# Optimization experiments

Measured on AMD Instinct MI355X. Metric: run time of the kernel, lower is better.

## Reference

```python
import jax, jax.numpy as jnp
import numpy as np

B, A, E = 8192, 56, 128          # batch, num_altas (=tgt_len), embed_dim
H, HD = 4, 16                     # num_heads, head_dim = E // H // 2
LAMBDA_INIT = 0.7
EPS = 1e-5
SCALING = HD ** -0.5


def _conv1d(x, w, b):
    # x: [N, C_in, L], w: [C_out, C_in, K], 'same' padding for K=7
    y = jax.lax.conv_general_dilated(
        x, w, window_strides=(1,), padding=[(3, 3)],
        dimension_numbers=('NCH', 'OIH', 'NCH'))
    return y + b[None, :, None]


def _layernorm(v, w, b):
    m = jnp.mean(v, axis=-1, keepdims=True)
    var = jnp.mean(jnp.square(v - m), axis=-1, keepdims=True)
    return (v - m) * jax.lax.rsqrt(var + EPS) * w + b


def setup_inputs() -> dict:
    key = jax.random.key(0)
    ks = jax.random.split(key, 12)
    return {
        'x': jax.random.normal(ks[0], (B, A, E), dtype=jnp.float32),
        'w_emb': jax.random.normal(ks[1], (A, A, 7), dtype=jnp.float32) * 0.05,
        'b_emb': jnp.zeros((A,), dtype=jnp.float32),
        'w_atlas': jax.random.normal(ks[2], (E, E, 7), dtype=jnp.float32) * 0.03,
        'b_atlas': jnp.zeros((E,), dtype=jnp.float32),
        'w_k': jax.random.normal(ks[3], (E, E), dtype=jnp.float32) * 0.08,
        'qn_w': jnp.ones((HD,), dtype=jnp.float32),
        'qn_b': jnp.zeros((HD,), dtype=jnp.float32),
        'kn_w': jnp.ones((HD,), dtype=jnp.float32),
        'kn_b': jnp.zeros((HD,), dtype=jnp.float32),
        'lambda_q1': jax.random.normal(ks[4], (HD,), dtype=jnp.float32) * 0.1,
        'lambda_k1': jax.random.normal(ks[5], (HD,), dtype=jnp.float32) * 0.1,
        'lambda_q2': jax.random.normal(ks[6], (HD,), dtype=jnp.float32) * 0.1,
        'lambda_k2': jax.random.normal(ks[7], (HD,), dtype=jnp.float32) * 0.1,
    }


def reference(x, w_emb, b_emb, w_atlas, b_atlas, w_k,
              qn_w, qn_b, kn_w, kn_b,
              lambda_q1, lambda_k1, lambda_q2, lambda_k2):
    bsz, tgt_len, embed_dim = x.shape
    # query formation: conv over atlas channels, SiLU, conv over embed channels,
    # SiLU, mean-pool over atlas positions -> [B, 1, E]
    h = jax.nn.silu(_conv1d(x, w_emb, b_emb))                  # [B, A, E]
    h = jax.nn.silu(_conv1d(h.transpose(0, 2, 1), w_atlas, b_atlas))  # [B, E, A]
    q = jnp.mean(h, axis=2)[:, None, :]                         # [B, 1, E]

    k = jnp.einsum('ble,oe->blo', x, w_k)                       # [B, A, E]

    q = q.reshape(bsz, 1, 2 * H, HD)
    k = k.reshape(bsz, tgt_len, 2 * H, HD)
    q = _layernorm(q, qn_w, qn_b) * SCALING
    k = _layernorm(k, kn_w, kn_b)

    attn = jnp.einsum('bqhe,bkhe->bhqk', q, k)                  # [B, 2H, 1, A]
    attn = jax.nn.softmax(attn, axis=-1)

    lam1 = jnp.exp(jnp.sum(lambda_q1 * lambda_k1))
    lam2 = jnp.exp(jnp.sum(lambda_q2 * lambda_k2))
    lambda_full = lam1 - lam2 + LAMBDA_INIT

    attn = attn.reshape(bsz, H, 2, 1, tgt_len)
    diff = attn[:, :, 0] - lambda_full * attn[:, :, 1]          # [B, H, 1, A]
    out = jax.nn.softmax(diff, axis=-1).mean(axis=1)            # [B, 1, A]
    return out.reshape(bsz, -1)                                 # [B, A]
```

## Files before the change

kernel.cpp:

```cpp
#include <hip/hip_runtime.h>
#include <math.h>

#define A_DIM 56
#define E_DIM 128

typedef short short8 __attribute__((ext_vector_type(8)));
typedef float floatx4 __attribute__((ext_vector_type(4)));

#define XT_HI_B 0
#define XT_LO_B 19296
#define H_HI_B  0
#define H_LO_B  16864
#define XR_HI_B 0
#define XR_LO_B 15232
#define KM_B    0
#define Q_B     33728
#define QN_B    34240
#define LG_B    34752
#define DP_B    36672
#define LAM_B   38592
#define SMEM_B  38608

#define QF   (Q_B/4)
#define QNF  (QN_B/4)
#define LGF  (LG_B/4)
#define DPF  (DP_B/4)
#define LAMF (LAM_B/4)
#define KP2  132

#define W1H 0
#define W1L 28672
#define W2H 57344
#define W2L 172032
#define WKH 286720
#define WKL 303104
#define PREP_ELEMS 159744

__device__ __forceinline__ unsigned rne16(unsigned u) {
  return (u + 0x7FFFu + ((u >> 16) & 1u)) >> 16;
}
__device__ __forceinline__ unsigned pack_hi16(unsigned u0, unsigned u1) {
  return __builtin_amdgcn_perm(u1, u0, 0x07060302u);
}
__device__ __forceinline__ float silu_f(float v) { return v / (1.f + __expf(-v)); }

__global__ void prep_weights(const float* __restrict__ w_emb,
                             const float* __restrict__ w_atlas,
                             const float* __restrict__ w_k,
                             unsigned short* __restrict__ ws) {
  int idx = blockIdx.x * 256 + threadIdx.x;
  if (idx >= PREP_ELEMS) return;
  float v; int dst_hi, dst_lo;
  if (idx < 28672) {
    int tap = idx >> 12, kc = (idx >> 11) & 1, nt = (idx >> 9) & 3;
    int lm = (idx >> 5) & 15, lkg = (idx >> 3) & 3, jj = idx & 7;
    int a = nt * 16 + lm, ci = kc * 32 + lkg * 8 + jj;
    v = (a < A_DIM && ci < A_DIM) ? w_emb[(a * A_DIM + ci) * 7 + tap] : 0.f;
    dst_hi = W1H + idx; dst_lo = W1L + idx;
  } else if (idx < 143360) {
    int j = idx - 28672;
    int tap = j >> 14, kc = (j >> 12) & 3, mt = (j >> 9) & 7;
    int lm = (j >> 5) & 15, lkg = (j >> 3) & 3, jj = j & 7;
    int eo = mt * 16 + lm, ei = kc * 32 + lkg * 8 + jj;
    v = w_atlas[(eo * E_DIM + ei) * 7 + tap];
    dst_hi = W2H + j; dst_lo = W2L + j;
  } else {
    int j = idx - 143360;
    int kc = j >> 12, mt = (j >> 9) & 7;
    int lm = (j >> 5) & 15, lkg = (j >> 3) & 3, jj = j & 7;
    int o = mt * 16 + lm, e = kc * 32 + lkg * 8 + jj;
    v = w_k[o * E_DIM + e];
    dst_hi = WKH + j; dst_lo = WKL + j;
  }
  unsigned u = __float_as_uint(v);
  unsigned hi = rne16(u);
  float lof = v - __uint_as_float(hi << 16);
  unsigned lo = rne16(__float_as_uint(lof));
  ws[dst_hi] = (unsigned short)hi;
  ws[dst_lo] = (unsigned short)lo;
}

__global__ __launch_bounds__(256, 4)
void atlas_fused(const float* __restrict__ x,
                 const unsigned short* __restrict__ ws,
                 const float* __restrict__ b_emb, const float* __restrict__ b_atlas,
                 const float* __restrict__ qn_w,  const float* __restrict__ qn_b,
                 const float* __restrict__ kn_w,  const float* __restrict__ kn_b,
                 const float* __restrict__ lq1,   const float* __restrict__ lk1,
                 const float* __restrict__ lq2,   const float* __restrict__ lk2,
                 float* __restrict__ out)
{
  __shared__ __align__(16) unsigned char smem[SMEM_B];
  float* smf = (float*)smem;
  const int t = threadIdx.x;
  const int b = blockIdx.x;
  const int lane = t & 63;
  const int w = __builtin_amdgcn_readfirstlane(t >> 6);
  const int lm = lane & 15;
  const int lkg8 = (lane >> 4) * 8;
  const int lr = (lane >> 4) * 4;

  const float* xb = x + (size_t)b * (A_DIM * E_DIM);

  {
    uint4 z4 = make_uint4(0, 0, 0, 0);
    for (int i = t; i < 352; i += 256) {
      if (i < 268) {
        int arr = i & 1, row = i >> 1;
        *(uint4*)(smem + (arr ? XT_LO_B : XT_HI_B) + row * 144 + 112) = z4;
      } else {
        int j = i - 268;
        int arr = j / 42; j -= arr * 42;
        int rowi = j / 7, c = j - rowi * 7;
        int row = (rowi < 3) ? rowi : 128 + rowi;
        *(uint4*)(smem + (arr ? XT_LO_B : XT_HI_B) + row * 144 + c * 16) = z4;
      }
    }
    if (t == 0) {
      float s1 = 0.f, s2 = 0.f;
      for (int i = 0; i < 16; ++i) { s1 += lq1[i] * lk1[i]; s2 += lq2[i] * lk2[i]; }
      smf[LAMF] = expf(s1) - expf(s2) + 0.7f;
    }
    int ab = t & 15;
    if (ab < 14) {
#pragma unroll
      for (int p = 0; p < 2; ++p) {
        int eb = (t >> 4) + 16 * p;
        floatx4 r0 = *(const floatx4*)(xb + (4 * ab + 0) * 128 + 4 * eb);
        floatx4 r1 = *(const floatx4*)(xb + (4 * ab + 1) * 128 + 4 * eb);
        floatx4 r2 = *(const floatx4*)(xb + (4 * ab + 2) * 128 + 4 * eb);
        floatx4 r3 = *(const floatx4*)(xb + (4 * ab + 3) * 128 + 4 * eb);
#pragma unroll
        for (int j2 = 0; j2 < 4; ++j2) {
          unsigned u0 = __float_as_uint(r0[j2]);
          unsigned u1 = __float_as_uint(r1[j2]);
          unsigned u2 = __float_as_uint(r2[j2]);
          unsigned u3 = __float_as_uint(r3[j2]);
          float l0 = r0[j2] - __uint_as_float(u0 & 0xFFFF0000u);
          float l1 = r1[j2] - __uint_as_float(u1 & 0xFFFF0000u);
          float l2 = r2[j2] - __uint_as_float(u2 & 0xFFFF0000u);
          float l3 = r3[j2] - __uint_as_float(u3 & 0xFFFF0000u);
          int off = (4 * eb + j2 + 3) * 144 + 8 * ab;
          *(uint2*)(smem + XT_HI_B + off) =
              make_uint2(pack_hi16(u0, u1), pack_hi16(u2, u3));
          *(uint2*)(smem + XT_LO_B + off) =
              make_uint2(pack_hi16(__float_as_uint(l0), __float_as_uint(l1)),
                         pack_hi16(__float_as_uint(l2), __float_as_uint(l3)));
        }
      }
    }
  }
  __syncthreads();

  {
    floatx4 acc[2][4];
#pragma unroll
    for (int nt = 0; nt < 4; ++nt) {
      int a = nt * 16 + lm;
      float be = (a < A_DIM) ? b_emb[a] : 0.f;
#pragma unroll
      for (int mt = 0; mt < 2; ++mt) {
        acc[mt][nt][0] = be; acc[mt][nt][1] = be;
        acc[mt][nt][2] = be; acc[mt][nt][3] = be;
      }
    }
    const unsigned short* xh = (const unsigned short*)(smem + XT_HI_B);
    const unsigned short* xl = (const unsigned short*)(smem + XT_LO_B);
#pragma unroll 1
    for (int tap = 0; tap < 7; ++tap) {
      int arow0 = (32 * w + lm + tap) * 72;
      int arow1 = arow0 + 16 * 72;
#pragma unroll
      for (int kc = 0; kc < 2; ++kc) {
        int ko = kc * 32 + lkg8;
        const unsigned short* fb = ws + ((tap * 2 + kc) * 4) * 512 + lm * 32 + lkg8;
        short8 bh0 = *(const short8*)(fb + W1H);
        short8 bh1 = *(const short8*)(fb + W1H + 512);
        short8 bh2 = *(const short8*)(fb + W1H + 1024);
        short8 bh3 = *(const short8*)(fb + W1H + 1536);
        short8 bl0 = *(const short8*)(fb + W1L);
        short8 bl1 = *(const short8*)(fb + W1L + 512);
        short8 bl2 = *(const short8*)(fb + W1L + 1024);
        short8 bl3 = *(const short8*)(fb + W1L + 1536);
        short8 ah0 = *(const short8*)(xh + arow0 + ko);
        short8 ah1 = *(const short8*)(xh + arow1 + ko);
        short8 al0 = *(const short8*)(xl + arow0 + ko);
        short8 al1 = *(const short8*)(xl + arow1 + ko);
        short8 bh[4] = {bh0, bh1, bh2, bh3};
        short8 bl[4] = {bl0, bl1, bl2, bl3};
#pragma unroll
        for (int nt = 0; nt < 4; ++nt) {
          acc[0][nt] = __builtin_amdgcn_mfma_f32_16x16x32_bf16(ah0, bh[nt], acc[0][nt], 0, 0, 0);
          acc[0][nt] = __builtin_amdgcn_mfma_f32_16x16x32_bf16(al0, bh[nt], acc[0][nt], 0, 0, 0);
          acc[0][nt] = __builtin_amdgcn_mfma_f32_16x16x32_bf16(ah0, bl[nt], acc[0][nt], 0, 0, 0);
          acc[1][nt] = __builtin_amdgcn_mfma_f32_16x16x32_bf16(ah1, bh[nt], acc[1][nt], 0, 0, 0);
          acc[1][nt] = __builtin_amdgcn_mfma_f32_16x16x32_bf16(al1, bh[nt], acc[1][nt], 0, 0, 0);
          acc[1][nt] = __builtin_amdgcn_mfma_f32_16x16x32_bf16(ah1, bl[nt], acc[1][nt], 0, 0, 0);
        }
      }
    }
    __syncthreads();
    {
      uint4 z4 = make_uint4(0, 0, 0, 0);
      for (int i = t; i < 204; i += 256) {
        int arr = i / 102, j = i - arr * 102;
        int r6 = j / 17, c = j - r6 * 17;
        int row = (r6 < 3) ? r6 : 56 + r6;
        *(uint4*)(smem + (arr ? H_LO_B : H_HI_B) + row * 272 + c * 16) = z4;
      }
    }
#pragma unroll
    for (int mt = 0; mt < 2; ++mt) {
      int e0 = 16 * (2 * w + mt) + lr;
#pragma unroll
      for (int nt = 0; nt < 4; ++nt) {
        int a = 16 * nt + lm;
        if (a < A_DIM) {
          float v0 = silu_f(acc[mt][nt][0]), v1 = silu_f(acc[mt][nt][1]);
          float v2 = silu_f(acc[mt][nt][2]), v3 = silu_f(acc[mt][nt][3]);
          unsigned u0 = __float_as_uint(v0), u1 = __float_as_uint(v1);
          unsigned u2 = __float_as_uint(v2), u3 = __float_as_uint(v3);
          float l0 = v0 - __uint_as_float(u0 & 0xFFFF0000u);
          float l1 = v1 - __uint_as_float(u1 & 0xFFFF0000u);
          float l2 = v2 - __uint_as_float(u2 & 0xFFFF0000u);
          float l3 = v3 - __uint_as_float(u3 & 0xFFFF0000u);
          int off = (a + 3) * 272 + e0 * 2;
          *(uint2*)(smem + H_HI_B + off) = make_uint2(pack_hi16(u0, u1), pack_hi16(u2, u3));
          *(uint2*)(smem + H_LO_B + off) =
              make_uint2(pack_hi16(__float_as_uint(l0), __float_as_uint(l1)),
                         pack_hi16(__float_as_uint(l2), __float_as_uint(l3)));
        }
      }
    }
  }
  __syncthreads();

  {
    floatx4 acc[2][4];
#pragma unroll
    for (int mt = 0; mt < 2; ++mt) {
      int eo0 = 16 * (2 * w + mt) + lr;
      float c0 = b_atlas[eo0], c1 = b_atlas[eo0 + 1];
      float c2 = b_atlas[eo0 + 2], c3 = b_atlas[eo0 + 3];
#pragma unroll
      for (int nt = 0; nt < 4; ++nt) {
        acc[mt][nt][0] = c0; acc[mt][nt][1] = c1;
        acc[mt][nt][2] = c2; acc[mt][nt][3] = c3;
      }
    }
    const unsigned char* hh = smem + H_HI_B;
    const unsigned char* hl = smem + H_LO_B;
#pragma unroll 1
    for (int tap = 0; tap < 7; ++tap) {
      int rofs[4];
#pragma unroll
      for (int nt = 0; nt < 4; ++nt) {
        int r = 16 * nt + lm + tap;
        rofs[nt] = ((r > 61) ? 61 : r) * 272;
      }
#pragma unroll
      for (int kc = 0; kc < 4; ++kc) {
        int kob = (kc * 32 + lkg8) * 2;
        const unsigned short* fb = ws + ((tap * 4 + kc) * 8 + 2 * w) * 512 + lm * 32 + lkg8;
        short8 ah0 = *(const short8*)(fb + W2H);
        short8 ah1 = *(const short8*)(fb + W2H + 512);
        short8 al0 = *(const short8*)(fb + W2L);
        short8 al1 = *(const short8*)(fb + W2L + 512);
        short8 bh[4], bl[4];
#pragma unroll
        for (int nt = 0; nt < 4; ++nt) {
          bh[nt] = *(const short8*)(hh + rofs[nt] + kob);
          bl[nt] = *(const short8*)(hl + rofs[nt] + kob);
        }
#pragma unroll
        for (int nt = 0; nt < 4; ++nt) {
          acc[0][nt] = __builtin_amdgcn_mfma_f32_16x16x32_bf16(ah0, bh[nt], acc[0][nt], 0, 0, 0);
          acc[0][nt] = __builtin_amdgcn_mfma_f32_16x16x32_bf16(al0, bh[nt], acc[0][nt], 0, 0, 0);
          acc[0][nt] = __builtin_amdgcn_mfma_f32_16x16x32_bf16(ah0, bl[nt], acc[0][nt], 0, 0, 0);
          acc[1][nt] = __builtin_amdgcn_mfma_f32_16x16x32_bf16(ah1, bh[nt], acc[1][nt], 0, 0, 0);
          acc[1][nt] = __builtin_amdgcn_mfma_f32_16x16x32_bf16(al1, bh[nt], acc[1][nt], 0, 0, 0);
          acc[1][nt] = __builtin_amdgcn_mfma_f32_16x16x32_bf16(ah1, bl[nt], acc[1][nt], 0, 0, 0);
        }
      }
    }
#pragma unroll
    for (int mt = 0; mt < 2; ++mt) {
#pragma unroll
      for (int r = 0; r < 4; ++r) {
        float s = 0.f;
#pragma unroll
        for (int nt = 0; nt < 4; ++nt) {
          float v = silu_f(acc[mt][nt][r]);
          int a = 16 * nt + lm;
          s += (a < A_DIM) ? v : 0.f;
        }
        s += __shfl_xor(s, 1, 64);
        s += __shfl_xor(s, 2, 64);
        s += __shfl_xor(s, 4, 64);
        s += __shfl_xor(s, 8, 64);
        if (lm == 0) {
          int eo = 16 * (2 * w + mt) + lr + r;
          smf[QF + eo] = s * (1.f / 56.f);
        }
      }
    }
  }
  __syncthreads();

  if (t < 128) {
    float v = smf[QF + t];
    float s = v;
#pragma unroll
    for (int m = 1; m < 16; m <<= 1) s += __shfl_xor(s, m, 64);
    float mean = s * (1.f / 16.f);
    float d = v - mean;
    float s2 = d * d;
#pragma unroll
    for (int m = 1; m < 16; m <<= 1) s2 += __shfl_xor(s2, m, 64);
    float var = s2 * (1.f / 16.f);
    int dd = t & 15;
    float qn = d * rsqrtf(var + 1e-5f) * qn_w[dd] + qn_b[dd];
    smf[QNF + t] = qn * 0.25f;
  }
  for (int i = t; i < 1792; i += 256) {
    int a = i >> 5, e4 = i & 31;
    float4 v = *(const float4*)(xb + a * 128 + e4 * 4);
    unsigned u0 = __float_as_uint(v.x), u1 = __float_as_uint(v.y);
    unsigned u2 = __float_as_uint(v.z), u3 = __float_as_uint(v.w);
    float l0 = v.x - __uint_as_float(u0 & 0xFFFF0000u);
    float l1 = v.y - __uint_as_float(u1 & 0xFFFF0000u);
    float l2 = v.z - __uint_as_float(u2 & 0xFFFF0000u);
    float l3 = v.w - __uint_as_float(u3 & 0xFFFF0000u);
    int off = a * 272 + e4 * 8;
    *(uint2*)(smem + XR_HI_B + off) = make_uint2(pack_hi16(u0, u1), pack_hi16(u2, u3));
    *(uint2*)(smem + XR_LO_B + off) =
        make_uint2(pack_hi16(__float_as_uint(l0), __float_as_uint(l1)),
                   pack_hi16(__float_as_uint(l2), __float_as_uint(l3)));
  }
  __syncthreads();

  {
    floatx4 acc[2][4];
#pragma unroll
    for (int mt = 0; mt < 2; ++mt)
#pragma unroll
      for (int nt = 0; nt < 4; ++nt) {
        acc[mt][nt][0] = 0.f; acc[mt][nt][1] = 0.f;
        acc[mt][nt][2] = 0.f; acc[mt][nt][3] = 0.f;
      }
    const unsigned char* xrh = smem + XR_HI_B;
    const unsigned char* xrl = smem + XR_LO_B;
    int rofs[4];
#pragma unroll
    for (int nt = 0; nt < 4; ++nt) {
      int a = 16 * nt + lm;
      rofs[nt] = ((a > 55) ? 55 : a) * 272;
    }
#pragma unroll 1
    for (int kc = 0; kc < 4; ++kc) {
      int kob = (kc * 32 + lkg8) * 2;
      const unsigned short* fb = ws + (kc * 8 + 2 * w) * 512 + lm * 32 + lkg8;
      short8 ah0 = *(const short8*)(fb + WKH);
      short8 ah1 = *(const short8*)(fb + WKH + 512);
      short8 al0 = *(const short8*)(fb + WKL);
      short8 al1 = *(const short8*)(fb + WKL + 512);
      short8 bh[4], bl[4];
#pragma unroll
      for (int nt = 0; nt < 4; ++nt) {
        bh[nt] = *(const short8*)(xrh + rofs[nt] + kob);
        bl[nt] = *(const short8*)(xrl + rofs[nt] + kob);
      }
#pragma unroll
      for (int nt = 0; nt < 4; ++nt) {
        acc[0][nt] = __builtin_amdgcn_mfma_f32_16x16x32_bf16(ah0, bh[nt], acc[0][nt], 0, 0, 0);
        acc[0][nt] = __builtin_amdgcn_mfma_f32_16x16x32_bf16(al0, bh[nt], acc[0][nt], 0, 0, 0);
        acc[0][nt] = __builtin_amdgcn_mfma_f32_16x16x32_bf16(ah0, bl[nt], acc[0][nt], 0, 0, 0);
        acc[1][nt] = __builtin_amdgcn_mfma_f32_16x16x32_bf16(ah1, bh[nt], acc[1][nt], 0, 0, 0);
        acc[1][nt] = __builtin_amdgcn_mfma_f32_16x16x32_bf16(al1, bh[nt], acc[1][nt], 0, 0, 0);
        acc[1][nt] = __builtin_amdgcn_mfma_f32_16x16x32_bf16(ah1, bl[nt], acc[1][nt], 0, 0, 0);
      }
    }
    __syncthreads();
#pragma unroll
    for (int mt = 0; mt < 2; ++mt) {
      int o0 = 16 * (2 * w + mt) + lr;
#pragma unroll
      for (int nt = 0; nt < 4; ++nt) {
        int a = 16 * nt + lm;
        if (a < A_DIM)
          *(floatx4*)&smf[(KM_B / 4) + a * KP2 + o0] = acc[mt][nt];
      }
    }
  }
  __syncthreads();

  for (int r = 0; r < 2; ++r) {
    int task = t + r * 256;
    if (task < A_DIM * 8) {
      int a = task >> 3, h2 = task & 7;
      float kv[16];
      float s = 0.f;
#pragma unroll
      for (int d = 0; d < 16; ++d) { kv[d] = smf[(KM_B / 4) + a * KP2 + h2 * 16 + d]; s += kv[d]; }
      float mean = s * (1.f / 16.f);
      float s2 = 0.f;
#pragma unroll
      for (int d = 0; d < 16; ++d) { float dd = kv[d] - mean; s2 += dd * dd; }
      float rs = rsqrtf(s2 * (1.f / 16.f) + 1e-5f);
      float logit = 0.f;
#pragma unroll
      for (int d = 0; d < 16; ++d) {
        float kn = (kv[d] - mean) * rs * kn_w[d] + kn_b[d];
        logit += smf[QNF + h2 * 16 + d] * kn;
      }
      smf[LGF + h2 * 60 + a] = logit;
    }
  }
  __syncthreads();

  {
    int g = t >> 5;
    int l = t & 31;
    float v0 = smf[LGF + g * 60 + l];
    bool has1 = (l < A_DIM - 32);
    float v1 = has1 ? smf[LGF + g * 60 + 32 + l] : -1e30f;
    float m = fmaxf(v0, v1);
#pragma unroll
    for (int s = 1; s < 32; s <<= 1) m = fmaxf(m, __shfl_xor(m, s, 64));
    float e0 = expf(v0 - m);
    float e1 = has1 ? expf(v1 - m) : 0.f;
    float ssum = e0 + e1;
#pragma unroll
    for (int s = 1; s < 32; s <<= 1) ssum += __shfl_xor(ssum, s, 64);
    float inv = 1.f / ssum;
    smf[LGF + g * 60 + l] = e0 * inv;
    if (has1) smf[LGF + g * 60 + 32 + l] = e1 * inv;
  }
  __syncthreads();

  {
    int h = t >> 6;
    int a = t & 63;
    float lam = smf[LAMF];
    float dlog = -1e30f;
    if (a < A_DIM) {
      float p0 = smf[LGF + (2 * h) * 60 + a];
      float p1 = smf[LGF + (2 * h + 1) * 60 + a];
      dlog = p0 - lam * p1;
    }
    float m = dlog;
#pragma unroll
    for (int s = 1; s < 64; s <<= 1) m = fmaxf(m, __shfl_xor(m, s, 64));
    float e = (a < A_DIM) ? expf(dlog - m) : 0.f;
    float ss = e;
#pragma unroll
    for (int s = 1; s < 64; s <<= 1) ss += __shfl_xor(ss, s, 64);
    if (a < A_DIM) smf[DPF + h * 60 + a] = e / ss;
  }
  __syncthreads();

  if (t < A_DIM) {
    float r = 0.25f * (smf[DPF + t] + smf[DPF + 60 + t] +
                       smf[DPF + 120 + t] + smf[DPF + 180 + t]);
    out[(size_t)b * A_DIM + t] = r;
  }
}

extern "C" void kernel_launch(void* const* d_in, const int* in_sizes, int n_in,
                              void* d_out, int out_size, void* d_ws, size_t ws_size,
                              hipStream_t stream) {
  const float* x       = (const float*)d_in[0];
  const float* w_emb   = (const float*)d_in[1];
  const float* b_emb   = (const float*)d_in[2];
  const float* w_atlas = (const float*)d_in[3];
  const float* b_atlas = (const float*)d_in[4];
  const float* w_k     = (const float*)d_in[5];
  const float* qn_w    = (const float*)d_in[6];
  const float* qn_b    = (const float*)d_in[7];
  const float* kn_w    = (const float*)d_in[8];
  const float* kn_b    = (const float*)d_in[9];
  const float* lq1     = (const float*)d_in[10];
  const float* lk1     = (const float*)d_in[11];
  const float* lq2     = (const float*)d_in[12];
  const float* lk2     = (const float*)d_in[13];
  float* out = (float*)d_out;
  unsigned short* ws = (unsigned short*)d_ws;

  prep_weights<<<dim3((PREP_ELEMS + 255) / 256), dim3(256), 0, stream>>>(
      w_emb, w_atlas, w_k, ws);

  const int Bn = in_sizes[0] / (A_DIM * E_DIM);
  atlas_fused<<<dim3(Bn), dim3(256), 0, stream>>>(
      x, ws, b_emb, b_atlas, qn_w, qn_b, kn_w, kn_b,
      lq1, lk1, lq2, lk2, out);
}
```

Measured before the change: 806.1 us.

## Raise wave priority around MFMA loops, prefetch x early, fuse softmax stages

After: 793.3 us. About the same (-1.6%).

```diff
diff --git a/kernel.cpp b/kernel.cpp
--- a/kernel.cpp
+++ b/kernel.cpp
@@ -166,6 +166,7 @@
     }
     const unsigned short* xh = (const unsigned short*)(smem + XT_HI_B);
     const unsigned short* xl = (const unsigned short*)(smem + XT_LO_B);
+    __builtin_amdgcn_s_setprio(1);
 #pragma unroll 1
     for (int tap = 0; tap < 7; ++tap) {
       int arow0 = (32 * w + lm + tap) * 72;
@@ -199,6 +200,7 @@
         }
       }
     }
+    __builtin_amdgcn_s_setprio(0);
     __syncthreads();
     {
       uint4 z4 = make_uint4(0, 0, 0, 0);
@@ -250,6 +252,7 @@
     }
     const unsigned char* hh = smem + H_HI_B;
     const unsigned char* hl = smem + H_LO_B;
+    __builtin_amdgcn_s_setprio(1);
 #pragma unroll 1
     for (int tap = 0; tap < 7; ++tap) {
       int rofs[4];
@@ -283,6 +286,7 @@
         }
       }
     }
+    __builtin_amdgcn_s_setprio(0);
 #pragma unroll
     for (int mt = 0; mt < 2; ++mt) {
 #pragma unroll
@@ -305,6 +309,13 @@
       }
     }
   }
+  float4 vbuf[7];
+#pragma unroll
+  for (int ii = 0; ii < 7; ++ii) {
+    int i = t + ii * 256;
+    int a = i >> 5, e4 = i & 31;
+    vbuf[ii] = *(const float4*)(xb + a * 128 + e4 * 4);
+  }
   __syncthreads();
 
   if (t < 128) {
@@ -322,9 +333,11 @@
     float qn = d * rsqrtf(var + 1e-5f) * qn_w[dd] + qn_b[dd];
     smf[QNF + t] = qn * 0.25f;
   }
-  for (int i = t; i < 1792; i += 256) {
+#pragma unroll
+  for (int ii = 0; ii < 7; ++ii) {
+    int i = t + ii * 256;
     int a = i >> 5, e4 = i & 31;
-    float4 v = *(const float4*)(xb + a * 128 + e4 * 4);
+    float4 v = vbuf[ii];
     unsigned u0 = __float_as_uint(v.x), u1 = __float_as_uint(v.y);
     unsigned u2 = __float_as_uint(v.z), u3 = __float_as_uint(v.w);
     float l0 = v.x - __uint_as_float(u0 & 0xFFFF0000u);
@@ -356,6 +369,7 @@
       int a = 16 * nt + lm;
       rofs[nt] = ((a > 55) ? 55 : a) * 272;
     }
+    __builtin_amdgcn_s_setprio(1);
 #pragma unroll 1
     for (int kc = 0; kc < 4; ++kc) {
       int kob = (kc * 32 + lkg8) * 2;
@@ -380,6 +394,7 @@
         acc[1][nt] = __builtin_amdgcn_mfma_f32_16x16x32_bf16(ah1, bl[nt], acc[1][nt], 0, 0, 0);
       }
     }
+    __builtin_amdgcn_s_setprio(0);
     __syncthreads();
 #pragma unroll
     for (int mt = 0; mt < 2; ++mt) {
@@ -419,43 +434,37 @@
   __syncthreads();
 
   {
-    int g = t >> 5;
-    int l = t & 31;
-    float v0 = smf[LGF + g * 60 + l];
-    bool has1 = (l < A_DIM - 32);
-    float v1 = has1 ? smf[LGF + g * 60 + 32 + l] : -1e30f;
-    float m = fmaxf(v0, v1);
-#pragma unroll
-    for (int s = 1; s < 32; s <<= 1) m = fmaxf(m, __shfl_xor(m, s, 64));
-    float e0 = expf(v0 - m);
-    float e1 = has1 ? expf(v1 - m) : 0.f;
-    float ssum = e0 + e1;
-#pragma unroll
-    for (int s = 1; s < 32; s <<= 1) ssum += __shfl_xor(ssum, s, 64);
-    float inv = 1.f / ssum;
-    smf[LGF + g * 60 + l] = e0 * inv;
-    if (has1) smf[LGF + g * 60 + 32 + l] = e1 * inv;
-  }
-  __syncthreads();
-
-  {
     int h = t >> 6;
     int a = t & 63;
+    bool act = (a < A_DIM);
     float lam = smf[LAMF];
-    float dlog = -1e30f;
-    if (a < A_DIM) {
-      float p0 = smf[LGF + (2 * h) * 60 + a];
-      float p1 = smf[LGF + (2 * h + 1) * 60 + a];
-      dlog = p0 - lam * p1;
-    }
+    float l0 = act ? smf[LGF + (2 * h) * 60 + a] : -1e30f;
+    float l1 = act ? smf[LGF + (2 * h + 1) * 60 + a] : -1e30f;
+    float m0 = l0, m1 = l1;
+#pragma unroll
+    for (int s = 1; s < 64; s <<= 1) {
+      m0 = fmaxf(m0, __shfl_xor(m0, s, 64));
+      m1 = fmaxf(m1, __shfl_xor(m1, s, 64));
+    }
+    float e0 = act ? expf(l0 - m0) : 0.f;
+    float e1 = act ? expf(l1 - m1) : 0.f;
+    float s0 = e0, s1 = e1;
+#pragma unroll
+    for (int s = 1; s < 64; s <<= 1) {
+      s0 += __shfl_xor(s0, s, 64);
+      s1 += __shfl_xor(s1, s, 64);
+    }
+    float p0 = e0 * (1.f / s0);
+    float p1 = e1 * (1.f / s1);
+    float dlog = act ? (p0 - lam * p1) : -1e30f;
     float m = dlog;
 #pragma unroll
     for (int s = 1; s < 64; s <<= 1) m = fmaxf(m, __shfl_xor(m, s, 64));
-    float e = (a < A_DIM) ? expf(dlog - m) : 0.f;
+    float e = act ? expf(dlog - m) : 0.f;
     float ss = e;
 #pragma unroll
     for (int s = 1; s < 64; s <<= 1) ss += __shfl_xor(ss, s, 64);
-    if (a < A_DIM) smf[DPF + h * 60 + a] = e / ss;
+    if (act) smf[DPF + h * 60 + a] = e / ss;
   }
   __syncthreads();
 
```
